# Performance work log

Measured on AMD Instinct MI355X. Metric: run time of the kernel, lower is better.

Reference implementation:

```python
import math
import jax, jax.numpy as jnp
import numpy as np

B, T, DMODEL, NUM_HEADS = 2, 2048, 1024, 16
HEAD_DIM = DMODEL // NUM_HEADS
MAX_TIMESCALE = 10000.0


def _sinusoid_reversed(batch, length, dim):
    # SinusoidalPositionEmbedding with reverse_order=True, cache_steps=0, no clamp
    pos = jnp.arange(length - 1, -1, -1, dtype=jnp.float32)  # [T]
    n = dim // 2
    inv = jnp.exp(jnp.arange(n, dtype=jnp.float32) * (-math.log(MAX_TIMESCALE) / (n - 1)))
    st = pos[:, None] * inv[None, :]                          # [T, n]
    emb = jnp.concatenate([jnp.sin(st), jnp.cos(st)], axis=-1)  # [T, dim]
    return jnp.broadcast_to(emb[None], (batch, length, dim))


def _relative_shift(x):
    # x: [B, H, t, T]
    b, h, t, TT = x.shape
    x = jnp.pad(x, ((0, 0), (0, 0), (0, 0), (1, 0)))
    x = jnp.reshape(x, (b, h, TT + 1, t))[:, :, 1:, :]
    return jnp.reshape(x, (b, h, t, TT))


def setup_inputs() -> dict:
    key = jax.random.key(0)
    ks = jax.random.split(key, 16)
    s = 1.0 / math.sqrt(DMODEL)
    d = {
        'x': jax.random.normal(ks[0], (B, T, DMODEL), jnp.float32),
        'y': jax.random.normal(ks[1], (B, T, DMODEL), jnp.float32),
        'mask': jnp.ones((B, 1, T, T), jnp.float32),
        'Wq': jax.random.normal(ks[2], (DMODEL, DMODEL), jnp.float32) * s,
        'bq': jnp.zeros((DMODEL,), jnp.float32),
        'Wk': jax.random.normal(ks[3], (DMODEL, DMODEL), jnp.float32) * s,
        'bk': jnp.zeros((DMODEL,), jnp.float32),
        'Wv': jax.random.normal(ks[4], (DMODEL, DMODEL), jnp.float32) * s,
        'bv': jnp.zeros((DMODEL,), jnp.float32),
        'Wp': jax.random.normal(ks[5], (DMODEL, DMODEL), jnp.float32) * s,
        'bp': jnp.zeros((DMODEL,), jnp.float32),
        'r_w_bias': jax.random.normal(ks[6], (1, 1, NUM_HEADS, HEAD_DIM), jnp.float32) * 0.02,
        'r_r_bias': jax.random.normal(ks[7], (1, 1, NUM_HEADS, HEAD_DIM), jnp.float32) * 0.02,
        'Wo': jax.random.normal(ks[8], (DMODEL, DMODEL), jnp.float32) * s,
        'bo': jnp.zeros((DMODEL,), jnp.float32),
    }
    return d


def reference(x, y, mask, Wq, bq, Wk, bk, Wv, bv, Wp, bp, r_w_bias, r_r_bias, Wo, bo):
    b, t, _ = x.shape
    kv_t = y.shape[1]
    q = (x @ Wq + bq).reshape(b, t, NUM_HEADS, HEAD_DIM)
    k = (y @ Wk + bk).reshape(b, kv_t, NUM_HEADS, HEAD_DIM)
    v = (y @ Wv + bv).reshape(b, kv_t, NUM_HEADS, HEAD_DIM)

    # RelativePositionEmbedding attend_fn
    content = jnp.einsum('bthd,bThd->bhtT', q + r_w_bias, k)
    pe = _sinusoid_reversed(b, kv_t, DMODEL) @ Wp + bp          # [B, kv_t, D]
    pe = pe.reshape(b, kv_t, NUM_HEADS, HEAD_DIM)
    rel = jnp.einsum('bthd,bThd->bhtT', q + r_r_bias, pe)
    rel = _relative_shift(rel)
    attn = (content + rel) * (1.0 / math.sqrt(HEAD_DIM))
    attn = attn * mask - 1e10 * (1.0 - mask)
    p = jax.nn.softmax(attn, axis=-1)
    out = jnp.einsum('bhtT,bThd->bthd', p, v).reshape(b, t, DMODEL)
    return out @ Wo + bo
```

## Files before the change

### kernel.cpp

```cpp
#include <hip/hip_runtime.h>
#include <math.h>

typedef __bf16 bf16_t;
typedef __bf16 bf16x8 __attribute__((ext_vector_type(8)));
typedef __bf16 bf16x4 __attribute__((ext_vector_type(4)));
typedef float  f32x4  __attribute__((ext_vector_type(4)));

#define DEV __device__ __forceinline__

#define QSCALE 0.18033688011112042f
#define MASKF  1.4426950408889634e10f

DEV float fexp2(float x) {
#if __has_builtin(__builtin_amdgcn_exp2f)
  return __builtin_amdgcn_exp2f(x);
#else
  return __expf(x * 0.6931471805599453f);
#endif
}

DEV void gl_lds16(const bf16_t* g, bf16_t* l) {
  __builtin_amdgcn_global_load_lds(
      (const __attribute__((address_space(1))) void*)g,
      (__attribute__((address_space(3))) void*)l, 16, 0, 0);
}

DEV int clamp2047(int c) { return c < 0 ? 0 : (c > 2047 ? 2047 : c); }

DEV int perow(int p, int r) {
  int c = (p < 50) ? (p * 64 + r) : ((p - 66) * 64 + r);
  return clamp2047(c);
}
DEV int s1c(int d) { return d <= 1 ? 32 + d : (d == 2 ? 68 : 67 + d); }

__global__ void k_cast2(const float* __restrict__ a, const float* __restrict__ b,
                        bf16_t* __restrict__ da, bf16_t* __restrict__ db, int n4) {
  int idx = blockIdx.x * blockDim.x + threadIdx.x;
  int stride = gridDim.x * blockDim.x;
  for (int i = idx; i < 2 * n4; i += stride) {
    const float4 v = (i < n4) ? ((const float4*)a)[i] : ((const float4*)b)[i - n4];
    bf16_t* d = (i < n4) ? (da + (size_t)i * 4) : (db + (size_t)(i - n4) * 4);
    bf16x4 o;
    o[0] = (bf16_t)v.x; o[1] = (bf16_t)v.y; o[2] = (bf16_t)v.z; o[3] = (bf16_t)v.w;
    *(bf16x4*)d = o;
  }
}

__global__ __launch_bounds__(256) void k_transpose5(
    const float* __restrict__ W0, const float* __restrict__ W1,
    const float* __restrict__ W2, const float* __restrict__ W3,
    const float* __restrict__ W4,
    bf16_t* __restrict__ T0, bf16_t* __restrict__ T1, bf16_t* __restrict__ T2,
    bf16_t* __restrict__ T3, bf16_t* __restrict__ T4) {
  const float* W; bf16_t* Wt;
  switch (blockIdx.z) {
    case 0: W = W0; Wt = T0; break;
    case 1: W = W1; Wt = T1; break;
    case 2: W = W2; Wt = T2; break;
    case 3: W = W3; Wt = T3; break;
    default: W = W4; Wt = T4; break;
  }
  __shared__ float tile[64][65];
  int k0 = blockIdx.x * 64, n0 = blockIdx.y * 64;
  int r = threadIdx.x >> 2;
  int c0 = (threadIdx.x & 3) * 16;
  const float4* src = (const float4*)(W + (size_t)(k0 + r) * 1024 + n0 + c0);
#pragma unroll
  for (int i = 0; i < 4; ++i) {
    float4 v = src[i];
    tile[r][c0 + i * 4 + 0] = v.x;
    tile[r][c0 + i * 4 + 1] = v.y;
    tile[r][c0 + i * 4 + 2] = v.z;
    tile[r][c0 + i * 4 + 3] = v.w;
  }
  __syncthreads();
#pragma unroll
  for (int half = 0; half < 2; ++half) {
    bf16x8 o;
#pragma unroll
    for (int j = 0; j < 8; ++j) o[j] = (bf16_t)tile[c0 + half * 8 + j][r];
    *(bf16x8*)(Wt + (size_t)(n0 + r) * 1024 + k0 + c0 + half * 8) = o;
  }
}

__global__ void k_sinusoid(bf16_t* __restrict__ tab) {
  int i = blockIdx.x;
  int d = threadIdx.x;
  float pos = (float)(2047 - i);
  const float coef = (float)(-9.210340371976184 / 511.0);
  float inv = expf((float)d * coef);
  float st = pos * inv;
  tab[(size_t)i * 1024 + d]       = (bf16_t)sinf(st);
  tab[(size_t)i * 1024 + 512 + d] = (bf16_t)cosf(st);
}

DEV void gemm_body(const bf16_t* __restrict__ A, const bf16_t* __restrict__ Bt,
                   const float* __restrict__ bias, const float* __restrict__ ebias,
                   float scale, bf16_t* __restrict__ outB, float* __restrict__ outF,
                   int m0, int n0, bf16_t* As, bf16_t* Bs) {
  const int tid = threadIdx.x;
  const int w = tid >> 6, lane = tid & 63, li = lane & 15, g = lane >> 4;
  const int mb = (w >> 1) * 64, nb = (w & 1) * 64;
  f32x4 acc[4][4] = {};
  for (int kt = 0; kt < 16; ++kt) {
    __syncthreads();
#pragma unroll
    for (int it = 0; it < 4; ++it) {
      int chunk = it * 256 + tid;
      int r = chunk >> 3, kg = chunk & 7;
      gl_lds16(A + (size_t)(m0 + r) * 1024 + kt * 64 + kg * 8, &As[chunk * 8]);
      gl_lds16(Bt + (size_t)(n0 + r) * 1024 + kt * 64 + kg * 8, &Bs[chunk * 8]);
    }
    __syncthreads();
#pragma unroll
    for (int kk = 0; kk < 64; kk += 32) {
      bf16x8 a[4], b[4];
#pragma unroll
      for (int x = 0; x < 4; ++x) {
        a[x] = *(const bf16x8*)&As[(mb + x * 16 + li) * 64 + kk + g * 8];
        b[x] = *(const bf16x8*)&Bs[(nb + x * 16 + li) * 64 + kk + g * 8];
      }
#pragma unroll
      for (int mr = 0; mr < 4; ++mr)
#pragma unroll
        for (int nr = 0; nr < 4; ++nr)
          acc[mr][nr] = __builtin_amdgcn_mfma_f32_16x16x32_bf16(a[mr], b[nr], acc[mr][nr], 0, 0, 0);
    }
  }
#pragma unroll
  for (int mr = 0; mr < 4; ++mr)
#pragma unroll
    for (int nr = 0; nr < 4; ++nr)
#pragma unroll
      for (int r4 = 0; r4 < 4; ++r4) {
        int row = m0 + mb + mr * 16 + g * 4 + r4;
        int col = n0 + nb + nr * 16 + li;
        float v = acc[mr][nr][r4] + bias[col];
        if (ebias) v += ebias[col];
        v *= scale;
        size_t off = (size_t)row * 1024 + col;
        if (outB) outB[off] = (bf16_t)v;
        if (outF) outF[off] = v;
      }
}

__global__ __launch_bounds__(256) void k_gemm(
    const bf16_t* __restrict__ A, const bf16_t* __restrict__ Bt,
    const float* __restrict__ bias, const float* __restrict__ ebias, float scale,
    bf16_t* __restrict__ outB, float* __restrict__ outF) {
  __shared__ bf16_t As[128 * 64];
  __shared__ bf16_t Bs[128 * 64];
  gemm_body(A, Bt, bias, ebias, scale, outB, outF,
            blockIdx.x * 128, blockIdx.y * 128, As, Bs);
}

__global__ __launch_bounds__(256) void k_gemm3(
    const bf16_t* __restrict__ xb, const bf16_t* __restrict__ yb,
    const bf16_t* __restrict__ Wqt, const bf16_t* __restrict__ Wkt,
    const bf16_t* __restrict__ Wvt,
    const float* __restrict__ bq, const float* __restrict__ bk,
    const float* __restrict__ bv, const float* __restrict__ rwb,
    bf16_t* __restrict__ qwb, bf16_t* __restrict__ kbuf, bf16_t* __restrict__ vbuf) {
  __shared__ bf16_t As[128 * 64];
  __shared__ bf16_t Bs[128 * 64];
  const int z = blockIdx.z;
  const bf16_t* A  = z == 0 ? xb : yb;
  const bf16_t* Bt = z == 0 ? Wqt : (z == 1 ? Wkt : Wvt);
  const float* bias = z == 0 ? bq : (z == 1 ? bk : bv);
  const float* eb   = z == 0 ? rwb : nullptr;
  float scale       = z == 0 ? QSCALE : 1.f;
  bf16_t* outB      = z == 0 ? qwb : (z == 1 ? kbuf : vbuf);
  gemm_body(A, Bt, bias, eb, scale, outB, nullptr,
            blockIdx.x * 128, blockIdx.y * 128, As, Bs);
}

__global__ __launch_bounds__(512, 2) void k_attn(
    const bf16_t* __restrict__ qw, const bf16_t* __restrict__ kb,
    const bf16_t* __restrict__ vb, const bf16_t* __restrict__ peb,
    const float* __restrict__ rwb, const float* __restrict__ rrb,
    const float* __restrict__ mask, bf16_t* __restrict__ attnb) {
  const int orig = blockIdx.x;
  const int xcd  = orig & 7;
  const int idx  = orig >> 3;
  const int pair = xcd * 4 + (idx >> 4);
  const int tb   = idx & 15;
  const int t0   = tb * 128;
  const int h    = pair & 15;
  const int b    = pair >> 4;
  const int tid = threadIdx.x;
  const int w = tid >> 6, lane = tid & 63, li = lane & 15, g = lane >> 4;

  __shared__ __align__(16) bf16_t k_s[64 * 72];
  __shared__ __align__(16) bf16_t vt_s[64 * 72];
  __shared__ __align__(16) bf16_t pe_s[4 * 64 * 64];
  __shared__ __align__(16) bf16_t p_all[8][16 * 72];

  bf16_t* p_w = &p_all[w][0];

  const size_t base_bh = (size_t)b * 2048 * 1024 + (size_t)h * 64;
  const int d0 = -2 * tb;

  {
    int r = tid >> 3, cc = tid & 7, ccs = cc ^ (r & 7);
#pragma unroll
    for (int q = 0; q < 2; ++q) {
      int p = 30 + d0 + q;
      gl_lds16(peb + (size_t)perow(p, r) * 1024 + h * 64 + ccs * 8,
               &pe_s[(p & 3) * 4096 + tid * 8]);
    }
  }
  bf16x8 pra, prb;
  {
    int r = tid >> 3, cc = tid & 7;
    pra = *(const bf16x8*)(peb + (size_t)perow(32 + d0, r) * 1024 + h * 64 + cc * 8);
    prb = pra;
  }

  bf16x8 kpf, vpf;
  {
    int r = tid >> 3, s = tid & 7;
    kpf = *(const bf16x8*)(kb + base_bh + (size_t)r * 1024 + s * 8);
    vpf = *(const bf16x8*)(vb + base_bh + (size_t)r * 1024 + s * 8);
  }

  bf16x8 aq[2], arA[2], arB[2];
  {
    int rowA = t0 + w * 16 + li;
    int rowB = rowA + 1 < 2048 ? rowA + 1 : 2047;
#pragma unroll
    for (int kkh = 0; kkh < 2; ++kkh) {
      int cof = kkh * 32 + g * 8;
      aq[kkh] = *(const bf16x8*)(qw + base_bh + (size_t)rowA * 1024 + cof);
      bf16x8 qb = *(const bf16x8*)(qw + base_bh + (size_t)rowB * 1024 + cof);
#pragma unroll
      for (int j = 0; j < 8; ++j) {
        float dj = (rrb[h * 64 + cof + j] - rwb[h * 64 + cof + j]) * QSCALE;
        arA[kkh][j] = (bf16_t)((float)aq[kkh][j] + dj);
        arB[kkh][j] = (bf16_t)((float)qb[j] + dj);
      }
    }
  }

  float mpf[4][4];
#pragma unroll
  for (int ct = 0; ct < 4; ++ct)
#pragma unroll
    for (int r4 = 0; r4 < 4; ++r4)
      mpf[ct][r4] = mask[((size_t)b * 2048 + t0 + w * 16 + g * 4 + r4) * 2048 + ct * 16 + li];

  float mrun[4], lrun[4];
  f32x4 oacc[4] = {};
#pragma unroll
  for (int r4 = 0; r4 < 4; ++r4) { mrun[r4] = -1e30f; lrun[r4] = 0.f; }

  for (int jt = 0; jt < 32; ++jt) {
    const int j0 = jt * 64;
    const int d = jt + d0;
    __syncthreads();
    {
      int r = tid >> 3, s = tid & 7;
      *(bf16x8*)&k_s[r * 72 + s * 8] = kpf;
      int up = (r >> 3) ^ s;
#pragma unroll
      for (int dd = 0; dd < 8; ++dd)
        vt_s[(s * 8 + dd) * 72 + up * 8 + (r & 7)] = vpf[dd];
      int p = s1c(d);
      int eo = (s ^ (r & 7)) * 8;
      *(bf16x8*)&pe_s[(p & 3) * 4096 + r * 64 + eo] = pra;
      if (d == 2) *(bf16x8*)&pe_s[(69 & 3) * 4096 + r * 64 + eo] = prb;
    }
    __syncthreads();

    f32x4 sc[4] = {};
#pragma unroll
    for (int kkh = 0; kkh < 2; ++kkh)
#pragma unroll
      for (int ct = 0; ct < 4; ++ct) {
        bf16x8 bk = *(const bf16x8*)&k_s[(ct * 16 + li) * 72 + kkh * 32 + g * 8];
        sc[ct] = __builtin_amdgcn_mfma_f32_16x16x32_bf16(aq[kkh], bk, sc[ct], 0, 0, 0);
      }

    const int sdc = j0 - t0 - w * 16;
#pragma unroll
    for (int cs = 0; cs < 2; ++cs) {
      const bool act = cs == 0 ? (sdc <= 15) : (sdc >= -61);
      if (!act) continue;
      const int c0 = cs ? (j0 - t0 - 129) : (1920 + j0 - t0);
      const bool bGlob = cs && (d <= 3);
      f32x4 ra[5] = {};
#pragma unroll
      for (int kkh = 0; kkh < 2; ++kkh) {
        bf16x8 a = cs ? arB[kkh] : arA[kkh];
#pragma unroll
        for (int f = 0; f < 5; ++f) {
          int c = c0 + (7 - w + f) * 16 + li;
          bf16x8 bpv;
          if (bGlob) {
            bpv = *(const bf16x8*)(peb + (size_t)clamp2047(c) * 1024 + h * 64 + kkh * 32 + g * 8);
          } else {
            int slot = cs ? (((c >> 6) + 2) & 3) : ((c >> 6) & 3);
            const char* pp = (const char*)pe_s + slot * 8192 + (c & 63) * 128 +
                             ((kkh * 64 + g * 16) ^ ((c & 7) << 4));
            bpv = *(const bf16x8*)pp;
            if (cs && w == 7 && f == 0) {
              bf16x8 vg = *(const bf16x8*)(peb + (size_t)clamp2047(c0) * 1024 + h * 64 + kkh * 32 + g * 8);
              if (li == 0) bpv = vg;
            }
          }
          ra[f] = __builtin_amdgcn_mfma_f32_16x16x32_bf16(a, bpv, ra[f], 0, 0, 0);
        }
      }
#pragma unroll
      for (int r4 = 0; r4 < 4; ++r4) {
        const int il = g * 4 + r4;
        const int srcLane = (lane & 48) | ((li - il + 15) & 15);
        float sh[5];
#pragma unroll
        for (int f = 0; f < 5; ++f) sh[f] = __shfl(ra[f][r4], srcLane, 64);
#pragma unroll
        for (int ct = 0; ct < 4; ++ct) {
          float rv = (li > il) ? sh[ct + 1] : sh[ct];
          int sd = sdc + ct * 16 + li - il;
          bool pr = cs ? (sd >= 2) : (sd <= 0);
          sc[ct][r4] += pr ? rv : 0.f;
        }
      }
    }

    if (jt < 31) {
      int r = tid >> 3, s = tid & 7;
      kpf = *(const bf16x8*)(kb + base_bh + (size_t)(j0 + 64 + r) * 1024 + s * 8);
      vpf = *(const bf16x8*)(vb + base_bh + (size_t)(j0 + 64 + r) * 1024 + s * 8);
      int pn = s1c(d + 1);
      pra = *(const bf16x8*)(peb + (size_t)perow(pn, r) * 1024 + h * 64 + s * 8);
      if (d + 1 == 2)
        prb = *(const bf16x8*)(peb + (size_t)perow(69, r) * 1024 + h * 64 + s * 8);
    }

    float rmax[4] = {-3e38f, -3e38f, -3e38f, -3e38f};
#pragma unroll
    for (int ct = 0; ct < 4; ++ct)
#pragma unroll
      for (int r4 = 0; r4 < 4; ++r4) {
        float s = fmaf(mpf[ct][r4] - 1.f, MASKF, sc[ct][r4]);
        sc[ct][r4] = s;
        rmax[r4] = fmaxf(rmax[r4], s);
      }
    {
      int j0n = j0 + 64; if (j0n > 1984) j0n = 1984;
#pragma unroll
      for (int ct = 0; ct < 4; ++ct)
#pragma unroll
        for (int r4 = 0; r4 < 4; ++r4)
          mpf[ct][r4] = mask[((size_t)b * 2048 + t0 + w * 16 + g * 4 + r4) * 2048 + j0n + ct * 16 + li];
    }
#pragma unroll
    for (int r4 = 0; r4 < 4; ++r4)
#pragma unroll
      for (int off = 1; off < 16; off <<= 1)
        rmax[r4] = fmaxf(rmax[r4], __shfl_xor(rmax[r4], off));
    float scl[4], rsum[4];
#pragma unroll
    for (int r4 = 0; r4 < 4; ++r4) {
      float mnew = fmaxf(mrun[r4], rmax[r4]);
      scl[r4] = fexp2(mrun[r4] - mnew);
      mrun[r4] = mnew;
      rsum[r4] = 0.f;
    }
#pragma unroll
    for (int ct = 0; ct < 4; ++ct)
#pragma unroll
      for (int r4 = 0; r4 < 4; ++r4) {
        float p = fexp2(sc[ct][r4] - mrun[r4]);
        sc[ct][r4] = p;
        rsum[r4] += p;
      }
#pragma unroll
    for (int r4 = 0; r4 < 4; ++r4) {
#pragma unroll
      for (int off = 1; off < 16; off <<= 1)
        rsum[r4] += __shfl_xor(rsum[r4], off);
      lrun[r4] = lrun[r4] * scl[r4] + rsum[r4];
    }
#pragma unroll
    for (int ct = 0; ct < 4; ++ct)
#pragma unroll
      for (int r4 = 0; r4 < 4; ++r4) oacc[ct][r4] *= scl[r4];

#pragma unroll
    for (int ct = 0; ct < 4; ++ct)
#pragma unroll
      for (int r4 = 0; r4 < 4; ++r4)
        p_w[(g * 4 + r4) * 72 + ct * 16 + li] = (bf16_t)sc[ct][r4];

#pragma unroll
    for (int kkh = 0; kkh < 2; ++kkh) {
      bf16x8 ap = *(const bf16x8*)&p_w[li * 72 + kkh * 32 + g * 8];
#pragma unroll
      for (int ct = 0; ct < 4; ++ct) {
        int dd = ct * 16 + li;
        int u2 = (kkh * 4 + g) ^ (dd >> 3);
        bf16x8 bv = *(const bf16x8*)&vt_s[dd * 72 + u2 * 8];
        oacc[ct] = __builtin_amdgcn_mfma_f32_16x16x32_bf16(ap, bv, oacc[ct], 0, 0, 0);
      }
    }
  }

#pragma unroll
  for (int ct = 0; ct < 4; ++ct)
#pragma unroll
    for (int r4 = 0; r4 < 4; ++r4) {
      int row = t0 + w * 16 + g * 4 + r4;
      float o = oacc[ct][r4] / lrun[r4];
      attnb[base_bh + (size_t)row * 1024 + ct * 16 + li] = (bf16_t)o;
    }
}

extern "C" void kernel_launch(void* const* d_in, const int* in_sizes, int n_in,
                              void* d_out, int out_size, void* d_ws, size_t ws_size,
                              hipStream_t stream) {
  (void)in_sizes; (void)n_in; (void)out_size; (void)ws_size;
  const float* x    = (const float*)d_in[0];
  const float* y    = (const float*)d_in[1];
  const float* mask = (const float*)d_in[2];
  const float* Wq   = (const float*)d_in[3];
  const float* bq   = (const float*)d_in[4];
  const float* Wk   = (const float*)d_in[5];
  const float* bk   = (const float*)d_in[6];
  const float* Wv   = (const float*)d_in[7];
  const float* bv   = (const float*)d_in[8];
  const float* Wp   = (const float*)d_in[9];
  const float* bp   = (const float*)d_in[10];
  const float* rwb  = (const float*)d_in[11];
  const float* rrb  = (const float*)d_in[12];
  const float* Wo   = (const float*)d_in[13];
  const float* bo   = (const float*)d_in[14];
  float* out = (float*)d_out;

  char* ws = (char*)d_ws;
  bf16_t* xb   = (bf16_t*)(ws + 0);
  bf16_t* yb   = (bf16_t*)(ws + (8ll << 20));
  bf16_t* Wqt  = (bf16_t*)(ws + (16ll << 20));
  bf16_t* Wkt  = (bf16_t*)(ws + (18ll << 20));
  bf16_t* Wvt  = (bf16_t*)(ws + (20ll << 20));
  bf16_t* Wpt  = (bf16_t*)(ws + (22ll << 20));
  bf16_t* Wot  = (bf16_t*)(ws + (24ll << 20));
  bf16_t* sint = (bf16_t*)(ws + (26ll << 20));
  bf16_t* qwb  = (bf16_t*)(ws + (30ll << 20));
  bf16_t* kbuf = (bf16_t*)(ws + (46ll << 20));
  bf16_t* vbuf = (bf16_t*)(ws + (54ll << 20));
  bf16_t* peb  = (bf16_t*)(ws + (62ll << 20));
  bf16_t* attnb = xb;

  k_cast2<<<2048, 256, 0, stream>>>(x, y, xb, yb, 1048576);
  k_transpose5<<<dim3(16, 16, 5), 256, 0, stream>>>(Wq, Wk, Wv, Wp, Wo,
                                                    Wqt, Wkt, Wvt, Wpt, Wot);
  k_sinusoid<<<2048, 512, 0, stream>>>(sint);

  k_gemm3<<<dim3(32, 8, 3), 256, 0, stream>>>(xb, yb, Wqt, Wkt, Wvt,
                                              bq, bk, bv, rwb, qwb, kbuf, vbuf);
  k_gemm<<<dim3(16, 8), 256, 0, stream>>>(sint, Wpt, bp, nullptr, 1.f, peb, nullptr);

  k_attn<<<512, 512, 0, stream>>>(qwb, kbuf, vbuf, peb, rwb, rrb, mask, attnb);

  k_gemm<<<dim3(32, 8), 256, 0, stream>>>(attnb, Wot, bo, nullptr, 1.f, nullptr, out);
}
```

Measured before the change: 319.6 us.

## Double-buffer K/V tiles via direct global-to-LDS loads with pre-transposed V

Adds a kernel that writes V in a transposed per-head layout so the attention loop can stream K and V^T straight into double-buffered LDS with async global_load_lds. This removes the per-iteration register staging, the scattered element-wise V transpose into shared memory and one of two barriers per tile. The PE ring buffer grows from 4 to 8 slots so staging the next tile's positional rows no longer collides with reads of the current tile. Row max and sum reductions now use DPP lane swaps instead of shfl_xor. The cost is an extra kernel launch with its own global pass over V, and more LDS per block, which may reduce occupancy.

```diff
diff --git a/kernel.cpp b/kernel.cpp
--- a/kernel.cpp
+++ b/kernel.cpp
@@ -32,6 +32,25 @@
   return clamp2047(c);
 }
 DEV int s1c(int d) { return d <= 1 ? 32 + d : (d == 2 ? 68 : 67 + d); }
+
+template <int CTRL> DEV float dppf(float x) {
+  return __int_as_float(__builtin_amdgcn_update_dpp(
+      0, __float_as_int(x), CTRL, 0xf, 0xf, true));
+}
+DEV float red16_max(float x) {
+  x = fmaxf(x, dppf<0xB1>(x));
+  x = fmaxf(x, dppf<0x4E>(x));
+  x = fmaxf(x, dppf<0x141>(x));
+  x = fmaxf(x, dppf<0x140>(x));
+  return x;
+}
+DEV float red16_sum(float x) {
+  x += dppf<0xB1>(x);
+  x += dppf<0x4E>(x);
+  x += dppf<0x141>(x);
+  x += dppf<0x140>(x);
+  return x;
+}
 
 __global__ void k_cast2(const float* __restrict__ a, const float* __restrict__ b,
                         bf16_t* __restrict__ da, bf16_t* __restrict__ db, int n4) {
@@ -92,6 +111,25 @@
   float st = pos * inv;
   tab[(size_t)i * 1024 + d]       = (bf16_t)sinf(st);
   tab[(size_t)i * 1024 + 512 + d] = (bf16_t)cosf(st);
+}
+
+__global__ __launch_bounds__(256) void k_vt(const bf16_t* __restrict__ vbuf,
+                                            bf16_t* __restrict__ vtb) {
+  const int kv0 = blockIdx.x * 64;
+  const int bh  = blockIdx.y;
+  const int b = bh >> 4, h = bh & 15;
+  const int d    = threadIdx.x & 63;
+  const int kv16 = (threadIdx.x >> 6) * 16;
+  bf16x8 o0, o1;
+#pragma unroll
+  for (int j = 0; j < 8; ++j)
+    o0[j] = vbuf[((size_t)b * 2048 + kv0 + kv16 + j) * 1024 + h * 64 + d];
+#pragma unroll
+  for (int j = 0; j < 8; ++j)
+    o1[j] = vbuf[((size_t)b * 2048 + kv0 + kv16 + 8 + j) * 1024 + h * 64 + d];
+  size_t dst = ((size_t)bh * 64 + d) * 2048 + kv0 + kv16;
+  *(bf16x8*)(vtb + dst) = o0;
+  *(bf16x8*)(vtb + dst + 8) = o1;
 }
 
 DEV void gemm_body(const bf16_t* __restrict__ A, const bf16_t* __restrict__ Bt,
@@ -176,7 +214,7 @@
 
 __global__ __launch_bounds__(512, 2) void k_attn(
     const bf16_t* __restrict__ qw, const bf16_t* __restrict__ kb,
-    const bf16_t* __restrict__ vb, const bf16_t* __restrict__ peb,
+    const bf16_t* __restrict__ vtb, const bf16_t* __restrict__ peb,
     const float* __restrict__ rwb, const float* __restrict__ rrb,
     const float* __restrict__ mask, bf16_t* __restrict__ attnb) {
   const int orig = blockIdx.x;
@@ -190,38 +228,27 @@
   const int tid = threadIdx.x;
   const int w = tid >> 6, lane = tid & 63, li = lane & 15, g = lane >> 4;
 
-  __shared__ __align__(16) bf16_t k_s[64 * 72];
-  __shared__ __align__(16) bf16_t vt_s[64 * 72];
-  __shared__ __align__(16) bf16_t pe_s[4 * 64 * 64];
+  __shared__ __align__(16) bf16_t k2[2 * 4096];
+  __shared__ __align__(16) bf16_t vt2[2 * 4096];
+  __shared__ __align__(16) bf16_t pe_s[8 * 4096];
   __shared__ __align__(16) bf16_t p_all[8][16 * 72];
-
   bf16_t* p_w = &p_all[w][0];
 
   const size_t base_bh = (size_t)b * 2048 * 1024 + (size_t)h * 64;
+  const size_t vtbase  = (size_t)(b * 16 + h) * 64 * 2048;
   const int d0 = -2 * tb;
-
-  {
-    int r = tid >> 3, cc = tid & 7, ccs = cc ^ (r & 7);
-#pragma unroll
-    for (int q = 0; q < 2; ++q) {
-      int p = 30 + d0 + q;
-      gl_lds16(peb + (size_t)perow(p, r) * 1024 + h * 64 + ccs * 8,
-               &pe_s[(p & 3) * 4096 + tid * 8]);
-    }
-  }
-  bf16x8 pra, prb;
-  {
-    int r = tid >> 3, cc = tid & 7;
-    pra = *(const bf16x8*)(peb + (size_t)perow(32 + d0, r) * 1024 + h * 64 + cc * 8);
-    prb = pra;
-  }
-
-  bf16x8 kpf, vpf;
-  {
-    int r = tid >> 3, s = tid & 7;
-    kpf = *(const bf16x8*)(kb + base_bh + (size_t)r * 1024 + s * 8);
-    vpf = *(const bf16x8*)(vb + base_bh + (size_t)r * 1024 + s * 8);
-  }
+  const int r8 = tid >> 3, c8 = tid & 7, cs8 = c8 ^ (r8 & 7);
+
+#pragma unroll
+  for (int q = 0; q < 3; ++q) {
+    int p = 30 + d0 + q;
+    gl_lds16(peb + (size_t)perow(p, r8) * 1024 + h * 64 + cs8 * 8,
+             &pe_s[(p & 7) * 4096 + tid * 8]);
+  }
+  gl_lds16(kb + ((size_t)b * 2048 + r8) * 1024 + h * 64 + cs8 * 8, &k2[tid * 8]);
+  gl_lds16(vtb + vtbase + (size_t)r8 * 2048 + cs8 * 8, &vt2[tid * 8]);
+
+  bf16x8 pra = {}, prb = {};
 
   bf16x8 aq[2], arA[2], arB[2];
   {
@@ -253,30 +280,30 @@
 #pragma unroll
   for (int r4 = 0; r4 < 4; ++r4) { mrun[r4] = -1e30f; lrun[r4] = 0.f; }
 
+  __syncthreads();
+
   for (int jt = 0; jt < 32; ++jt) {
     const int j0 = jt * 64;
     const int d = jt + d0;
-    __syncthreads();
-    {
-      int r = tid >> 3, s = tid & 7;
-      *(bf16x8*)&k_s[r * 72 + s * 8] = kpf;
-      int up = (r >> 3) ^ s;
-#pragma unroll
-      for (int dd = 0; dd < 8; ++dd)
-        vt_s[(s * 8 + dd) * 72 + up * 8 + (r & 7)] = vpf[dd];
-      int p = s1c(d);
-      int eo = (s ^ (r & 7)) * 8;
-      *(bf16x8*)&pe_s[(p & 3) * 4096 + r * 64 + eo] = pra;
-      if (d == 2) *(bf16x8*)&pe_s[(69 & 3) * 4096 + r * 64 + eo] = prb;
-    }
-    __syncthreads();
+    const bf16_t* kC = &k2[(jt & 1) * 4096];
+    const bf16_t* vC = &vt2[(jt & 1) * 4096];
+
+    if (jt < 31) {
+      gl_lds16(kb + ((size_t)b * 2048 + j0 + 64 + r8) * 1024 + h * 64 + cs8 * 8,
+               &k2[((jt + 1) & 1) * 4096 + tid * 8]);
+      gl_lds16(vtb + vtbase + (size_t)r8 * 2048 + j0 + 64 + cs8 * 8,
+               &vt2[((jt + 1) & 1) * 4096 + tid * 8]);
+      pra = *(const bf16x8*)(peb + (size_t)perow(s1c(d + 1), r8) * 1024 + h * 64 + c8 * 8);
+      if (d == 2)
+        prb = *(const bf16x8*)(peb + (size_t)perow(69, r8) * 1024 + h * 64 + c8 * 8);
+    }
 
     f32x4 sc[4] = {};
 #pragma unroll
     for (int kkh = 0; kkh < 2; ++kkh)
 #pragma unroll
       for (int ct = 0; ct < 4; ++ct) {
-        bf16x8 bk = *(const bf16x8*)&k_s[(ct * 16 + li) * 72 + kkh * 32 + g * 8];
+        bf16x8 bk = *(const bf16x8*)&kC[(ct * 16 + li) * 64 + (((kkh * 4 + g) ^ (li & 7)) * 8)];
         sc[ct] = __builtin_amdgcn_mfma_f32_16x16x32_bf16(aq[kkh], bk, sc[ct], 0, 0, 0);
       }
 
@@ -298,7 +325,7 @@
           if (bGlob) {
             bpv = *(const bf16x8*)(peb + (size_t)clamp2047(c) * 1024 + h * 64 + kkh * 32 + g * 8);
           } else {
-            int slot = cs ? (((c >> 6) + 2) & 3) : ((c >> 6) & 3);
+            int slot = cs ? (((c >> 6) + 2) & 7) : ((c >> 6) & 7);
             const char* pp = (const char*)pe_s + slot * 8192 + (c & 63) * 128 +
                              ((kkh * 64 + g * 16) ^ ((c & 7) << 4));
             bpv = *(const bf16x8*)pp;
@@ -327,16 +354,6 @@
       }
     }
 
-    if (jt < 31) {
-      int r = tid >> 3, s = tid & 7;
-      kpf = *(const bf16x8*)(kb + base_bh + (size_t)(j0 + 64 + r) * 1024 + s * 8);
-      vpf = *(const bf16x8*)(vb + base_bh + (size_t)(j0 + 64 + r) * 1024 + s * 8);
-      int pn = s1c(d + 1);
-      pra = *(const bf16x8*)(peb + (size_t)perow(pn, r) * 1024 + h * 64 + s * 8);
-      if (d + 1 == 2)
-        prb = *(const bf16x8*)(peb + (size_t)perow(69, r) * 1024 + h * 64 + s * 8);
-    }
-
     float rmax[4] = {-3e38f, -3e38f, -3e38f, -3e38f};
 #pragma unroll
     for (int ct = 0; ct < 4; ++ct)
@@ -354,14 +371,10 @@
         for (int r4 = 0; r4 < 4; ++r4)
           mpf[ct][r4] = mask[((size_t)b * 2048 + t0 + w * 16 + g * 4 + r4) * 2048 + j0n + ct * 16 + li];
     }
-#pragma unroll
-    for (int r4 = 0; r4 < 4; ++r4)
-#pragma unroll
-      for (int off = 1; off < 16; off <<= 1)
-        rmax[r4] = fmaxf(rmax[r4], __shfl_xor(rmax[r4], off));
     float scl[4], rsum[4];
 #pragma unroll
     for (int r4 = 0; r4 < 4; ++r4) {
+      rmax[r4] = red16_max(rmax[r4]);
       float mnew = fmaxf(mrun[r4], rmax[r4]);
       scl[r4] = fexp2(mrun[r4] - mnew);
       mrun[r4] = mnew;
@@ -377,9 +390,7 @@
       }
 #pragma unroll
     for (int r4 = 0; r4 < 4; ++r4) {
-#pragma unroll
-      for (int off = 1; off < 16; off <<= 1)
-        rsum[r4] += __shfl_xor(rsum[r4], off);
+      rsum[r4] = red16_sum(rsum[r4]);
       lrun[r4] = lrun[r4] * scl[r4] + rsum[r4];
     }
 #pragma unroll
@@ -398,12 +409,17 @@
       bf16x8 ap = *(const bf16x8*)&p_w[li * 72 + kkh * 32 + g * 8];
 #pragma unroll
       for (int ct = 0; ct < 4; ++ct) {
-        int dd = ct * 16 + li;
-        int u2 = (kkh * 4 + g) ^ (dd >> 3);
-        bf16x8 bv = *(const bf16x8*)&vt_s[dd * 72 + u2 * 8];
+        bf16x8 bv = *(const bf16x8*)&vC[(ct * 16 + li) * 64 + (((kkh * 4 + g) ^ (li & 7)) * 8)];
         oacc[ct] = __builtin_amdgcn_mfma_f32_16x16x32_bf16(ap, bv, oacc[ct], 0, 0, 0);
       }
     }
+
+    if (jt < 31) {
+      int p = s1c(d + 1);
+      *(bf16x8*)&pe_s[(p & 7) * 4096 + r8 * 64 + cs8 * 8] = pra;
+      if (d == 2) *(bf16x8*)&pe_s[5 * 4096 + r8 * 64 + cs8 * 8] = prb;
+    }
+    __syncthreads();
   }
 
 #pragma unroll
@@ -450,6 +466,7 @@
   bf16_t* kbuf = (bf16_t*)(ws + (46ll << 20));
   bf16_t* vbuf = (bf16_t*)(ws + (54ll << 20));
   bf16_t* peb  = (bf16_t*)(ws + (62ll << 20));
+  bf16_t* vtb  = (bf16_t*)(ws + (66ll << 20));
   bf16_t* attnb = xb;
 
   k_cast2<<<2048, 256, 0, stream>>>(x, y, xb, yb, 1048576);
@@ -460,8 +477,9 @@
   k_gemm3<<<dim3(32, 8, 3), 256, 0, stream>>>(xb, yb, Wqt, Wkt, Wvt,
                                               bq, bk, bv, rwb, qwb, kbuf, vbuf);
   k_gemm<<<dim3(16, 8), 256, 0, stream>>>(sint, Wpt, bp, nullptr, 1.f, peb, nullptr);
-
-  k_attn<<<512, 512, 0, stream>>>(qwb, kbuf, vbuf, peb, rwb, rrb, mask, attnb);
+  k_vt<<<dim3(32, 32), 256, 0, stream>>>(vbuf, vtb);
+
+  k_attn<<<512, 512, 0, stream>>>(qwb, kbuf, vtb, peb, rwb, rrb, mask, attnb);
 
   k_gemm<<<dim3(32, 8), 256, 0, stream>>>(attnb, Wot, bo, nullptr, 1.f, nullptr, out);
 }
```

After: 308.4 us. 1.04x faster.
